# Performance work log

Measured on AMD Instinct MI355X. Metric: run time of the kernel, lower is better.

## Reference

```python
import jax, jax.numpy as jnp
import numpy as np

B, D, F, H = 256, 9, 8, 256   # batch of trees, tree depth, input features, hidden
N = 2 ** (D + 1) - 1          # total nodes per full binary tree (heap layout)


def _init(key, shape, fan_in):
    return jax.random.normal(key, shape, jnp.float32) * (1.0 / np.sqrt(fan_in))


def setup_inputs() -> dict:
    key = jax.random.key(0)
    ks = jax.random.split(key, 6)
    return {
        "data": jax.random.normal(ks[0], (B, N, F), jnp.float32),
        "Wu": _init(ks[1], (H, F), F),
        "bu": jnp.zeros((H,), jnp.float32),
        "Wr": _init(ks[2], (3 * H, 3 * H), 3 * H),
        "br": jnp.zeros((3 * H,), jnp.float32),
        "Wh": _init(ks[3], (H, 3 * H), 3 * H),
        "bh": jnp.zeros((H,), jnp.float32),
        "Wz": _init(ks[4], (4 * H, 4 * H), 4 * H),
        "bz": jnp.zeros((4 * H,), jnp.float32),
        "Wp": _init(ks[5], (1, H), H),
        "bp": jnp.zeros((1,), jnp.float32),
    }


def reference(data, Wu, bu, Wr, br, Wh, bh, Wz, bz, Wp, bp):
    # data: [B, N, F] node features in heap (level-order) layout;
    # children of the i-th node of level l are nodes 2i, 2i+1 of level l+1.
    b, n_nodes, _ = data.shape
    L = (n_nodes + 1) // 2          # number of leaves
    depth = L.bit_length() - 1
    h_dim = Wu.shape[0]

    # leaf embedding u for every node (leaf() is applied at every tree node)
    u = jnp.einsum('bnf,hf->bnh', data, Wu) + bu          # [B, N, H]
    h = u[:, L - 1:, :]                                    # leaf level states [B, L, H]

    for l in range(depth - 1, -1, -1):                     # bottom-up over levels
        n = 2 ** l
        parent = u[:, n - 1:2 * n - 1, :]                  # [B, n, H]
        h_l, h_r = h[:, 0::2, :], h[:, 1::2, :]            # [B, n, H] each
        hhu = jnp.concatenate([parent, h_l, h_r], axis=-1)  # [B, n, 3H]
        r = jax.nn.sigmoid(jnp.einsum('bnk,jk->bnj', hhu, Wr) + br)
        h_new = jax.nn.relu(jnp.einsum('bnk,hk->bnh', r * hhu, Wh) + bh)
        hhhu = jnp.concatenate([h_new, hhu], axis=-1)      # [B, n, 4H]
        zlin = jnp.einsum('bnk,jk->bnj', hhhu, Wz) + bz    # [B, n, 4H]
        z = jax.nn.softmax(zlin.reshape(b, n, 4, h_dim), axis=2)
        h = (z * hhhu.reshape(b, n, 4, h_dim)).sum(axis=2)  # gated combine -> [B, n, H]

    # h is [B, 1, H] at the root; logits head
    logits = jnp.einsum('bnh,oh->bno', h, Wp) + bp          # [B, 1, 1]
    return logits[:, 0, 0]                                  # [B]
```

## Files before the change

kernel.cpp:

```cpp
#include <hip/hip_runtime.h>
#include <math.h>

#define BB 256
#define NN 1023
#define FF 8
#define HH 256
#define DEPTH 9

enum { EPI_NONE = 0, EPI_SIGMUL = 1, EPI_RELU = 2, EPI_COMBINE = 3 };

typedef __bf16 bf16x8_t __attribute__((ext_vector_type(8)));
typedef float f32x4_t __attribute__((ext_vector_type(4)));

__device__ __forceinline__ void stage16(const void* g, void* l) {
    __builtin_amdgcn_global_load_lds(
        (const __attribute__((address_space(1))) void*)g,
        (__attribute__((address_space(3))) void*)l,
        16, 0, 0);
}

__device__ __forceinline__ int xcd_remap(int hw, int nwg) {
    const int xcd = hw & 7, k0 = hw >> 3;
    const int qq = nwg >> 3, rr = nwg & 7;
    return (xcd < rr ? xcd * (qq + 1) : rr * (qq + 1) + (xcd - rr) * qq) + k0;
}

template <int EPI>
__global__ __launch_bounds__(512, 1) void gemm256p(
    const __bf16* __restrict__ A, int lda,
    const __bf16* __restrict__ W,
    const float* __restrict__ bias,
    const __bf16* __restrict__ aux, int ldaux,
    void* __restrict__ Cout, int ldc,
    int K)
{
    __shared__ __bf16 lds[2][2][256 * 64];
    const int tid = threadIdx.x;
    const int lane = tid & 63;
    const int w = tid >> 6;
    const int wr = w >> 2, wc = w & 3;

    const int nwg = gridDim.x * gridDim.y;
    const int hw = blockIdx.y * gridDim.x + blockIdx.x;
    const int wg = xcd_remap(hw, nwg);
    const int bm0 = (wg / gridDim.x) * 256;
    const int bn0 = (wg % gridDim.x) * 256;

    const int srow = tid >> 3;
    const int scolz = ((tid & 7) ^ (srow & 7)) * 8;

    f32x4_t acc[8][4];
#pragma unroll
    for (int i = 0; i < 8; ++i)
#pragma unroll
        for (int j = 0; j < 4; ++j) acc[i][j] = (f32x4_t){0.f, 0.f, 0.f, 0.f};

    const int rA = lane & 15;
    const int klane = (lane >> 4) * 8;
    const int rxor = (lane & 7) * 8;
    const int NT = K >> 6;

#define STAGE_A_Q(t, buf, q)                                                   \
    do {                                                                       \
        const int kk_ = (t) << 6;                                              \
        stage16(A + (size_t)(bm0 + (q) * 64 + srow) * lda + kk_ + scolz,       \
                &lds[buf][0][((q) * 64) * 64 + w * 512]);                      \
        stage16(A + (size_t)(bm0 + 128 + (q) * 64 + srow) * lda + kk_ + scolz, \
                &lds[buf][0][((128 + (q) * 64)) * 64 + w * 512]);              \
    } while (0)
#define STAGE_B_H(t, buf, hf)                                                  \
    do {                                                                       \
        const int kk_ = (t) << 6;                                              \
        stage16(W + (size_t)(bn0 + (hf) * 128 + srow) * K + kk_ + scolz,       \
                &lds[buf][1][((hf) * 128) * 64 + w * 512]);                    \
        stage16(W + (size_t)(bn0 + (hf) * 128 + 64 + srow) * K + kk_ + scolz,  \
                &lds[buf][1][((hf) * 128 + 64) * 64 + w * 512]);               \
    } while (0)

#define LDA_F(As_, i, ks) \
    (*(const bf16x8_t*)&(As_)[(wr * 128 + (i) * 16 + rA) * 64 + (((ks) * 32 + klane) ^ rxor)])
#define LDB_F(Bs_, j, ks) \
    (*(const bf16x8_t*)&(Bs_)[(wc * 64 + (j) * 16 + rA) * 64 + (((ks) * 32 + klane) ^ rxor)])

    STAGE_A_Q(0, 0, 0);
    STAGE_B_H(0, 0, 0);
    STAGE_B_H(0, 0, 1);
    STAGE_A_Q(0, 0, 1);
    asm volatile("s_waitcnt vmcnt(2)" ::: "memory");
    __builtin_amdgcn_s_barrier();

    for (int t = 0; t < NT; ++t) {
        const int c = t & 1, n = c ^ 1;
        const __bf16* As = lds[c][0];
        const __bf16* Bs = lds[c][1];
        const bool more = (t + 1 < NT);
        bf16x8_t a0[4], a1[4], b0[4], b1[4];

#pragma unroll
        for (int j = 0; j < 4; ++j) b0[j] = LDB_F(Bs, j, 0);
#pragma unroll
        for (int i = 0; i < 4; ++i) a0[i] = LDA_F(As, i, 0);
        if (more) STAGE_A_Q(t + 1, n, 0);
        __builtin_amdgcn_s_barrier();
        asm volatile("s_waitcnt lgkmcnt(0)" ::: "memory");
        __builtin_amdgcn_s_setprio(1);
#pragma unroll
        for (int i = 0; i < 4; ++i)
#pragma unroll
            for (int j = 0; j < 4; ++j)
                acc[i][j] = __builtin_amdgcn_mfma_f32_16x16x32_bf16(
                    a0[i], b0[j], acc[i][j], 0, 0, 0);
        __builtin_amdgcn_s_setprio(0);
        __builtin_amdgcn_s_barrier();

#pragma unroll
        for (int j = 0; j < 4; ++j) b1[j] = LDB_F(Bs, j, 1);
#pragma unroll
        for (int i = 0; i < 4; ++i) a1[i] = LDA_F(As, i, 1);
        if (more) STAGE_B_H(t + 1, n, 0);
        __builtin_amdgcn_s_barrier();
        asm volatile("s_waitcnt lgkmcnt(0)" ::: "memory");
        __builtin_amdgcn_s_setprio(1);
#pragma unroll
        for (int i = 0; i < 4; ++i)
#pragma unroll
            for (int j = 0; j < 4; ++j)
                acc[i][j] = __builtin_amdgcn_mfma_f32_16x16x32_bf16(
                    a1[i], b1[j], acc[i][j], 0, 0, 0);
        __builtin_amdgcn_s_setprio(0);
        if (more) {
            asm volatile("s_waitcnt vmcnt(4)" ::: "memory");
        } else {
            asm volatile("s_waitcnt vmcnt(0)" ::: "memory");
        }
        __builtin_amdgcn_s_barrier();

#pragma unroll
        for (int i = 0; i < 4; ++i) a0[i] = LDA_F(As, 4 + i, 0);
        if (more) STAGE_B_H(t + 1, n, 1);
        __builtin_amdgcn_s_barrier();
        asm volatile("s_waitcnt lgkmcnt(0)" ::: "memory");
        __builtin_amdgcn_s_setprio(1);
#pragma unroll
        for (int i = 0; i < 4; ++i)
#pragma unroll
            for (int j = 0; j < 4; ++j)
                acc[4 + i][j] = __builtin_amdgcn_mfma_f32_16x16x32_bf16(
                    a0[i], b0[j], acc[4 + i][j], 0, 0, 0);
        __builtin_amdgcn_s_setprio(0);
        __builtin_amdgcn_s_barrier();

#pragma unroll
        for (int i = 0; i < 4; ++i) a1[i] = LDA_F(As, 4 + i, 1);
        if (more) STAGE_A_Q(t + 1, n, 1);
        __builtin_amdgcn_s_barrier();
        asm volatile("s_waitcnt lgkmcnt(0)" ::: "memory");
        __builtin_amdgcn_s_setprio(1);
#pragma unroll
        for (int i = 0; i < 4; ++i)
#pragma unroll
            for (int j = 0; j < 4; ++j)
                acc[4 + i][j] = __builtin_amdgcn_mfma_f32_16x16x32_bf16(
                    a1[i], b1[j], acc[4 + i][j], 0, 0, 0);
        __builtin_amdgcn_s_setprio(0);
        if (more) {
            asm volatile("s_waitcnt vmcnt(2)" ::: "memory");
            __builtin_amdgcn_s_barrier();
        }
    }
#undef STAGE_A_Q
#undef STAGE_B_H
#undef LDA_F
#undef LDB_F

    if (EPI == EPI_COMBINE) {
        const int r = lane & 15;
        const int G = ((bn0 + wc * 64) >> 2) + r;
        float bz4[4];
#pragma unroll
        for (int g = 0; g < 4; ++g) bz4[g] = bias[bn0 + wc * 64 + g * 16 + r];
#pragma unroll
        for (int i = 0; i < 8; ++i) {
#pragma unroll
            for (int reg = 0; reg < 4; ++reg) {
                const int gr = bm0 + wr * 128 + i * 16 + (lane >> 4) * 4 + reg;
                float z0 = acc[i][0][reg] + bz4[0];
                float z1 = acc[i][1][reg] + bz4[1];
                float z2 = acc[i][2][reg] + bz4[2];
                float z3 = acc[i][3][reg] + bz4[3];
                float mx = fmaxf(fmaxf(z0, z1), fmaxf(z2, z3));
                float e0 = __expf(z0 - mx), e1 = __expf(z1 - mx);
                float e2 = __expf(z2 - mx), e3 = __expf(z3 - mx);
                const __bf16* hrow = aux + (size_t)gr * ldaux + G;
                float hv = (e0 * (float)hrow[0] + e1 * (float)hrow[256] +
                            e2 * (float)hrow[512] + e3 * (float)hrow[768]) /
                           (e0 + e1 + e2 + e3);
                ((__bf16*)Cout)[(size_t)gr * ldc + G] = (__bf16)hv;
            }
        }
    } else {
#pragma unroll
        for (int j = 0; j < 4; ++j) {
            const int gc = bn0 + wc * 64 + j * 16 + (lane & 15);
            const float bv = bias[gc];
#pragma unroll
            for (int i = 0; i < 8; ++i) {
#pragma unroll
                for (int reg = 0; reg < 4; ++reg) {
                    const int gr = bm0 + wr * 128 + i * 16 + (lane >> 4) * 4 + reg;
                    float v = acc[i][j][reg] + bv;
                    if (EPI == EPI_SIGMUL) {
                        float s = 1.0f / (1.0f + __expf(-v));
                        v = s * (float)aux[(size_t)gr * ldaux + gc];
                        ((__bf16*)Cout)[(size_t)gr * ldc + gc] = (__bf16)v;
                    } else if (EPI == EPI_RELU) {
                        v = fmaxf(v, 0.0f);
                        ((__bf16*)Cout)[(size_t)gr * ldc + gc] = (__bf16)v;
                    } else {
                        ((float*)Cout)[(size_t)gr * ldc + gc] = v;
                    }
                }
            }
        }
    }
}

template <int EPI>
__global__ __launch_bounds__(256) void gemm_mfma(
    const __bf16* __restrict__ A, int lda,
    const __bf16* __restrict__ W,
    const float* __restrict__ bias,
    const __bf16* __restrict__ aux, int ldaux,
    void* __restrict__ Cout, int ldc,
    int K)
{
    __shared__ __bf16 As[128 * 32];
    __shared__ __bf16 Bs[128 * 32];
    const int tid = threadIdx.x;
    const int lane = tid & 63;
    const int w = tid >> 6;
    const int wr = w >> 1, wc = w & 1;

    const int nwg = gridDim.x * gridDim.y;
    const int hw = blockIdx.y * gridDim.x + blockIdx.x;
    const int wg = xcd_remap(hw, nwg);
    const int bm0 = (wg / gridDim.x) * 128;
    const int bn0 = (wg % gridDim.x) * 128;

    const int srow = lane >> 2;
    const int scol = (lane & 3) * 8;

    f32x4_t acc[4][4];
#pragma unroll
    for (int i = 0; i < 4; ++i)
#pragma unroll
        for (int j = 0; j < 4; ++j) acc[i][j] = (f32x4_t){0.f, 0.f, 0.f, 0.f};

    const int rA = lane & 15;
    const int kslot = (lane >> 4) * 8;

    for (int kk = 0; kk < K; kk += 32) {
        stage16(A + (size_t)(bm0 + w * 16 + srow) * lda + kk + scol,
                &As[(w * 16) * 32]);
        stage16(A + (size_t)(bm0 + 64 + w * 16 + srow) * lda + kk + scol,
                &As[(64 + w * 16) * 32]);
        stage16(W + (size_t)(bn0 + w * 16 + srow) * K + kk + scol,
                &Bs[(w * 16) * 32]);
        stage16(W + (size_t)(bn0 + 64 + w * 16 + srow) * K + kk + scol,
                &Bs[(64 + w * 16) * 32]);
        __syncthreads();

        bf16x8_t af[4], bfr[4];
#pragma unroll
        for (int i = 0; i < 4; ++i)
            af[i] = *(const bf16x8_t*)&As[(wr * 64 + i * 16 + rA) * 32 + kslot];
#pragma unroll
        for (int j = 0; j < 4; ++j)
            bfr[j] = *(const bf16x8_t*)&Bs[(wc * 64 + j * 16 + rA) * 32 + kslot];
#pragma unroll
        for (int i = 0; i < 4; ++i)
#pragma unroll
            for (int j = 0; j < 4; ++j)
                acc[i][j] = __builtin_amdgcn_mfma_f32_16x16x32_bf16(
                    af[i], bfr[j], acc[i][j], 0, 0, 0);
        __syncthreads();
    }

    if (EPI == EPI_COMBINE) {
        const int r = lane & 15;
        const int G = ((bn0 + wc * 64) >> 2) + r;
        float bz4[4];
#pragma unroll
        for (int g = 0; g < 4; ++g) bz4[g] = bias[bn0 + wc * 64 + g * 16 + r];
#pragma unroll
        for (int i = 0; i < 4; ++i) {
#pragma unroll
            for (int reg = 0; reg < 4; ++reg) {
                const int gr = bm0 + wr * 64 + i * 16 + (lane >> 4) * 4 + reg;
                float z0 = acc[i][0][reg] + bz4[0];
                float z1 = acc[i][1][reg] + bz4[1];
                float z2 = acc[i][2][reg] + bz4[2];
                float z3 = acc[i][3][reg] + bz4[3];
                float mx = fmaxf(fmaxf(z0, z1), fmaxf(z2, z3));
                float e0 = __expf(z0 - mx), e1 = __expf(z1 - mx);
                float e2 = __expf(z2 - mx), e3 = __expf(z3 - mx);
                const __bf16* hrow = aux + (size_t)gr * ldaux + G;
                float hv = (e0 * (float)hrow[0] + e1 * (float)hrow[256] +
                            e2 * (float)hrow[512] + e3 * (float)hrow[768]) /
                           (e0 + e1 + e2 + e3);
                ((__bf16*)Cout)[(size_t)gr * ldc + G] = (__bf16)hv;
            }
        }
    } else {
#pragma unroll
        for (int j = 0; j < 4; ++j) {
            const int gc = bn0 + wc * 64 + j * 16 + (lane & 15);
            const float bv = bias[gc];
#pragma unroll
            for (int i = 0; i < 4; ++i) {
#pragma unroll
                for (int reg = 0; reg < 4; ++reg) {
                    const int gr = bm0 + wr * 64 + i * 16 + (lane >> 4) * 4 + reg;
                    float v = acc[i][j][reg] + bv;
                    if (EPI == EPI_SIGMUL) {
                        float s = 1.0f / (1.0f + __expf(-v));
                        v = s * (float)aux[(size_t)gr * ldaux + gc];
                        ((__bf16*)Cout)[(size_t)gr * ldc + gc] = (__bf16)v;
                    } else if (EPI == EPI_RELU) {
                        v = fmaxf(v, 0.0f);
                        ((__bf16*)Cout)[(size_t)gr * ldc + gc] = (__bf16)v;
                    } else {
                        ((float*)Cout)[(size_t)gr * ldc + gc] = v;
                    }
                }
            }
        }
    }
}

__global__ __launch_bounds__(256) void convert_weights(
    const float* __restrict__ Wr, const float* __restrict__ Wh,
    const float* __restrict__ Wz, const float* __restrict__ bz,
    __bf16* __restrict__ Wrb, __bf16* __restrict__ Whb,
    __bf16* __restrict__ Wzb, float* __restrict__ bzp)
{
    const int NR = 768 * 768, NH2 = 256 * 768, NZ = 1024 * 1024;
    const int idx0 = blockIdx.x * 256 + threadIdx.x;
    for (int i = idx0; i < NR + NH2 + NZ; i += gridDim.x * 256) {
        if (i < NR) Wrb[i] = (__bf16)Wr[i];
        else if (i < NR + NH2) Whb[i - NR] = (__bf16)Wh[i - NR];
        else {
            const int z = i - NR - NH2;
            const int p = z >> 10, k = z & 1023;
            const int o = ((p >> 4) & 3) * 256 + (p >> 6) * 16 + (p & 15);
            Wzb[z] = (__bf16)Wz[(size_t)o * 1024 + k];
        }
    }
    if (idx0 < 1024) {
        const int p = idx0;
        const int o = ((p >> 4) & 3) * 256 + (p >> 6) * 16 + (p & 15);
        bzp[p] = bz[o];
    }
}

__global__ __launch_bounds__(256) void build_hhu(
    const float* __restrict__ data, const float* __restrict__ Wu,
    const float* __restrict__ bu, const __bf16* __restrict__ hprev,
    __bf16* __restrict__ hhhu, int l, int r0)
{
    const int n = 1 << l;
    const int blk = xcd_remap(blockIdx.x, gridDim.x);
    const int row = blk * 8 + (threadIdx.x >> 5);
    const int c0 = (threadIdx.x & 31) * 8;
    const int i = r0 + row;
    const int b = i >> l;
    const int m = i & (n - 1);

    float wv[8][8];
#pragma unroll
    for (int cc = 0; cc < 8; ++cc) {
        float4 w0 = *(const float4*)&Wu[(c0 + cc) * 8];
        float4 w1 = *(const float4*)&Wu[(c0 + cc) * 8 + 4];
        wv[cc][0] = w0.x; wv[cc][1] = w0.y; wv[cc][2] = w0.z; wv[cc][3] = w0.w;
        wv[cc][4] = w1.x; wv[cc][5] = w1.y; wv[cc][6] = w1.z; wv[cc][7] = w1.w;
    }
    float buv[8];
#pragma unroll
    for (int cc = 0; cc < 8; ++cc) buv[cc] = bu[c0 + cc];

    __bf16* rowp = hhhu + (size_t)row * 1024;

    {
        const float* dp = data + ((size_t)b * NN + (n - 1) + m) * FF;
        float4 d0 = *(const float4*)dp, d1 = *(const float4*)(dp + 4);
        float dv[8] = {d0.x, d0.y, d0.z, d0.w, d1.x, d1.y, d1.z, d1.w};
        bf16x8_t o;
#pragma unroll
        for (int cc = 0; cc < 8; ++cc) {
            float acc = buv[cc];
#pragma unroll
            for (int f = 0; f < 8; ++f) acc += dv[f] * wv[cc][f];
            o[cc] = (__bf16)acc;
        }
        *(bf16x8_t*)&rowp[256 + c0] = o;
    }

    if (l == 8) {
        const float* dl = data + ((size_t)b * NN + 511 + 2 * m) * FF;
#pragma unroll
        for (int side = 0; side < 2; ++side) {
            const float* dp = dl + side * FF;
            float4 d0 = *(const float4*)dp, d1 = *(const float4*)(dp + 4);
            float dv[8] = {d0.x, d0.y, d0.z, d0.w, d1.x, d1.y, d1.z, d1.w};
            bf16x8_t o;
#pragma unroll
            for (int cc = 0; cc < 8; ++cc) {
                float acc = buv[cc];
#pragma unroll
                for (int f = 0; f < 8; ++f) acc += dv[f] * wv[cc][f];
                o[cc] = (__bf16)acc;
            }
            *(bf16x8_t*)&rowp[512 + side * 256 + c0] = o;
        }
    } else {
        *(bf16x8_t*)&rowp[512 + c0] =
            *(const bf16x8_t*)&hprev[((size_t)b * (2 * n) + 2 * m) * HH + c0];
        *(bf16x8_t*)&rowp[768 + c0] =
            *(const bf16x8_t*)&hprev[((size_t)b * (2 * n) + 2 * m + 1) * HH + c0];
    }
}

__global__ __launch_bounds__(256) void final_kernel(
    const __bf16* __restrict__ hfin, const float* __restrict__ Wp,
    const float* __restrict__ bp, float* __restrict__ out)
{
    const int b = blockIdx.x;
    const int t = threadIdx.x;
    __shared__ float red[256];
    red[t] = (float)hfin[(size_t)b * HH + t] * Wp[t];
    __syncthreads();
    for (int s = 128; s > 0; s >>= 1) {
        if (t < s) red[t] += red[t + s];
        __syncthreads();
    }
    if (t == 0) out[b] = red[0] + bp[0];
}

extern "C" void kernel_launch(void* const* d_in, const int* in_sizes, int n_in,
                              void* d_out, int out_size, void* d_ws, size_t ws_size,
                              hipStream_t stream)
{
    const float* data = (const float*)d_in[0];
    const float* Wu = (const float*)d_in[1];
    const float* bu = (const float*)d_in[2];
    const float* Wr = (const float*)d_in[3];
    const float* br = (const float*)d_in[4];
    const float* Wh = (const float*)d_in[5];
    const float* bh = (const float*)d_in[6];
    const float* Wz = (const float*)d_in[7];
    const float* bz = (const float*)d_in[8];
    const float* Wp = (const float*)d_in[9];
    const float* bp = (const float*)d_in[10];
    float* out = (float*)d_out;

    const size_t CAP = 32768;
    char* w = (char*)d_ws;
    __bf16* hA = (__bf16*)w;   w += (size_t)65536 * HH * 2;
    __bf16* hB = (__bf16*)w;   w += (size_t)32768 * HH * 2;
    __bf16* hhhu = (__bf16*)w; w += CAP * 1024 * 2;
    __bf16* rh = (__bf16*)w;   w += CAP * 768 * 2;
    __bf16* Wrb = (__bf16*)w;  w += (size_t)768 * 768 * 2;
    __bf16* Whb = (__bf16*)w;  w += (size_t)256 * 768 * 2;
    __bf16* Wzb = (__bf16*)w;  w += (size_t)1024 * 1024 * 2;
    float* bzp = (float*)w;    w += 1024 * 4;

    convert_weights<<<2048, 256, 0, stream>>>(Wr, Wh, Wz, bz, Wrb, Whb, Wzb, bzp);

    for (int l = DEPTH - 1; l >= 0; --l) {
        const size_t M = (size_t)BB << l;
        __bf16* dst = ((DEPTH - 1 - l) & 1) ? hB : hA;
        const __bf16* src = ((DEPTH - 1 - l) & 1) ? hA : hB;
        for (size_t r0 = 0; r0 < M; r0 += CAP) {
            const int R = (int)((M - r0 < CAP) ? (M - r0) : CAP);
            build_hhu<<<R / 8, 256, 0, stream>>>(data, Wu, bu, src, hhhu, l, (int)r0);
            if (R >= 2048) {
                gemm256p<EPI_SIGMUL><<<dim3(3, R / 256), 512, 0, stream>>>(
                    hhhu + 256, 1024, Wrb, br, hhhu + 256, 1024, rh, 768, 768);
            } else {
                gemm_mfma<EPI_SIGMUL><<<dim3(6, R / 128), 256, 0, stream>>>(
                    hhhu + 256, 1024, Wrb, br, hhhu + 256, 1024, rh, 768, 768);
            }
            gemm_mfma<EPI_RELU><<<dim3(2, R / 128), 256, 0, stream>>>(
                rh, 768, Whb, bh, nullptr, 0, hhhu, 1024, 768);
            if (R >= 2048) {
                gemm256p<EPI_COMBINE><<<dim3(4, R / 256), 512, 0, stream>>>(
                    hhhu, 1024, Wzb, bzp, hhhu, 1024,
                    dst + (size_t)r0 * HH, HH, 1024);
            } else {
                gemm_mfma<EPI_COMBINE><<<dim3(8, R / 128), 256, 0, stream>>>(
                    hhhu, 1024, Wzb, bzp, hhhu, 1024,
                    dst + (size_t)r0 * HH, HH, 1024);
            }
        }
    }
    final_kernel<<<BB, 256, 0, stream>>>(hA, Wp, bp, out);
}
```

Measured before the change: 1.250 ms.

## Fold Wu into Wr/Wz and gather GEMM A-operands directly from tree buffers

Precomputes folded weights so the parent-embedding term of the reset and gate GEMMs uses the 8 raw bf16 input features, padded to 64, instead of the 256-wide u vector. This cuts K from 768 to 576 and from 1024 to 832. The large-level GEMMs now gather A tiles straight from child hidden states, converted data and the new-h buffer, so the concatenated hhhu buffer is no longer built. Small levels keep the old path. The cost is irregular gather addressing and an extra bf16 rounding of the folded weights.

```diff
diff --git a/kernel.cpp b/kernel.cpp
--- a/kernel.cpp
+++ b/kernel.cpp
@@ -26,13 +26,34 @@
 }
 
 template <int EPI>
-__global__ __launch_bounds__(512, 1) void gemm256p(
-    const __bf16* __restrict__ A, int lda,
+__device__ __forceinline__ const __bf16* a_src(
+    int t, size_t gi, int l, int lrow, int scolz,
+    const __bf16* __restrict__ hprev, const __bf16* __restrict__ hnew,
+    const __bf16* __restrict__ dbf)
+{
+    const int b = (int)(gi >> l);
+    const int m = (int)gi & ((1 << l) - 1);
+    const size_t child = (((size_t)b) << (l + 1)) + 2 * m;
+    if (EPI == EPI_SIGMUL) {
+        if (t == 0) return dbf + ((size_t)b * NN + (1 << l) - 1 + m) * FF;
+        if (t <= 4) return hprev + child * HH + (t - 1) * 64 + scolz;
+        return hprev + (child + 1) * HH + (t - 5) * 64 + scolz;
+    } else {
+        if (t < 4) return hnew + (size_t)lrow * HH + t * 64 + scolz;
+        if (t == 4) return dbf + ((size_t)b * NN + (1 << l) - 1 + m) * FF;
+        if (t <= 8) return hprev + child * HH + (t - 5) * 64 + scolz;
+        return hprev + (child + 1) * HH + (t - 9) * 64 + scolz;
+    }
+}
+
+template <int EPI>
+__global__ __launch_bounds__(512, 1) void gemm256g(
+    const __bf16* __restrict__ hprev, const __bf16* __restrict__ ubuf,
+    const __bf16* __restrict__ hnew, const __bf16* __restrict__ dbf,
     const __bf16* __restrict__ W,
     const float* __restrict__ bias,
-    const __bf16* __restrict__ aux, int ldaux,
-    void* __restrict__ Cout, int ldc,
-    int K)
+    void* __restrict__ Cout,
+    int r0, int l, int K)
 {
     __shared__ __bf16 lds[2][2][256 * 64];
     const int tid = threadIdx.x;
@@ -48,6 +69,7 @@
 
     const int srow = tid >> 3;
     const int scolz = ((tid & 7) ^ (srow & 7)) * 8;
+    const int mask = (1 << l) - 1;
 
     f32x4_t acc[8][4];
 #pragma unroll
@@ -60,13 +82,17 @@
     const int rxor = (lane & 7) * 8;
     const int NT = K >> 6;
 
+#define STAGE_A_LINE(t, buf, rbase)                                            \
+    do {                                                                       \
+        const int lrow_ = bm0 + (rbase) + srow;                                \
+        const __bf16* s_ = a_src<EPI>((t), (size_t)r0 + lrow_, l, lrow_,       \
+                                      scolz, hprev, hnew, dbf);                \
+        stage16(s_, &lds[buf][0][(rbase) * 64 + w * 512]);                     \
+    } while (0)
 #define STAGE_A_Q(t, buf, q)                                                   \
     do {                                                                       \
-        const int kk_ = (t) << 6;                                              \
-        stage16(A + (size_t)(bm0 + (q) * 64 + srow) * lda + kk_ + scolz,       \
-                &lds[buf][0][((q) * 64) * 64 + w * 512]);                      \
-        stage16(A + (size_t)(bm0 + 128 + (q) * 64 + srow) * lda + kk_ + scolz, \
-                &lds[buf][0][((128 + (q) * 64)) * 64 + w * 512]);              \
+        STAGE_A_LINE(t, buf, (q) * 64);                                        \
+        STAGE_A_LINE(t, buf, 128 + (q) * 64);                                  \
     } while (0)
 #define STAGE_B_H(t, buf, hf)                                                  \
     do {                                                                       \
@@ -76,7 +102,6 @@
         stage16(W + (size_t)(bn0 + (hf) * 128 + 64 + srow) * K + kk_ + scolz,  \
                 &lds[buf][1][((hf) * 128 + 64) * 64 + w * 512]);               \
     } while (0)
-
 #define LDA_F(As_, i, ks) \
     (*(const bf16x8_t*)&(As_)[(wr * 128 + (i) * 16 + rA) * 64 + (((ks) * 32 + klane) ^ rxor)])
 #define LDB_F(Bs_, j, ks) \
@@ -90,7 +115,7 @@
     __builtin_amdgcn_s_barrier();
 
     for (int t = 0; t < NT; ++t) {
-        const int c = t & 1, n = c ^ 1;
+        const int c = t & 1, nb = c ^ 1;
         const __bf16* As = lds[c][0];
         const __bf16* Bs = lds[c][1];
         const bool more = (t + 1 < NT);
@@ -100,7 +125,7 @@
         for (int j = 0; j < 4; ++j) b0[j] = LDB_F(Bs, j, 0);
 #pragma unroll
         for (int i = 0; i < 4; ++i) a0[i] = LDA_F(As, i, 0);
-        if (more) STAGE_A_Q(t + 1, n, 0);
+        if (more) STAGE_A_Q(t + 1, nb, 0);
         __builtin_amdgcn_s_barrier();
         asm volatile("s_waitcnt lgkmcnt(0)" ::: "memory");
         __builtin_amdgcn_s_setprio(1);
@@ -117,7 +142,7 @@
         for (int j = 0; j < 4; ++j) b1[j] = LDB_F(Bs, j, 1);
 #pragma unroll
         for (int i = 0; i < 4; ++i) a1[i] = LDA_F(As, i, 1);
-        if (more) STAGE_B_H(t + 1, n, 0);
+        if (more) STAGE_B_H(t + 1, nb, 0);
         __builtin_amdgcn_s_barrier();
         asm volatile("s_waitcnt lgkmcnt(0)" ::: "memory");
         __builtin_amdgcn_s_setprio(1);
@@ -137,7 +162,7 @@
 
 #pragma unroll
         for (int i = 0; i < 4; ++i) a0[i] = LDA_F(As, 4 + i, 0);
-        if (more) STAGE_B_H(t + 1, n, 1);
+        if (more) STAGE_B_H(t + 1, nb, 1);
         __builtin_amdgcn_s_barrier();
         asm volatile("s_waitcnt lgkmcnt(0)" ::: "memory");
         __builtin_amdgcn_s_setprio(1);
@@ -152,7 +177,7 @@
 
 #pragma unroll
         for (int i = 0; i < 4; ++i) a1[i] = LDA_F(As, 4 + i, 1);
-        if (more) STAGE_A_Q(t + 1, n, 1);
+        if (more) STAGE_A_Q(t + 1, nb, 1);
         __builtin_amdgcn_s_barrier();
         asm volatile("s_waitcnt lgkmcnt(0)" ::: "memory");
         __builtin_amdgcn_s_setprio(1);
@@ -168,13 +193,40 @@
             __builtin_amdgcn_s_barrier();
         }
     }
+#undef STAGE_A_LINE
 #undef STAGE_A_Q
 #undef STAGE_B_H
 #undef LDA_F
 #undef LDB_F
 
-    if (EPI == EPI_COMBINE) {
-        const int r = lane & 15;
+    const int hi = lane >> 4;
+    const int r = lane & 15;
+
+    if (EPI == EPI_SIGMUL) {
+#pragma unroll
+        for (int j = 0; j < 4; ++j) {
+            const int gc = bn0 + wc * 64 + j * 16 + r;
+            const float bv = bias[gc];
+#pragma unroll
+            for (int i = 0; i < 8; ++i) {
+#pragma unroll
+                for (int reg = 0; reg < 4; ++reg) {
+                    const int gr = bm0 + wr * 128 + i * 16 + hi * 4 + reg;
+                    const size_t gi = (size_t)r0 + gr;
+                    const int b = (int)(gi >> l);
+                    const int m = (int)gi & mask;
+                    const size_t child = (((size_t)b) << (l + 1)) + 2 * m;
+                    float a;
+                    if (gc < 256) a = (float)ubuf[(size_t)gr * HH + gc];
+                    else if (gc < 512) a = (float)hprev[child * HH + gc - 256];
+                    else a = (float)hprev[(child + 1) * HH + gc - 512];
+                    float v = acc[i][j][reg] + bv;
+                    float s = 1.0f / (1.0f + __expf(-v));
+                    ((__bf16*)Cout)[(size_t)gr * 768 + gc] = (__bf16)(s * a);
+                }
+            }
+        }
+    } else {
         const int G = ((bn0 + wc * 64) >> 2) + r;
         float bz4[4];
 #pragma unroll
@@ -183,7 +235,11 @@
         for (int i = 0; i < 8; ++i) {
 #pragma unroll
             for (int reg = 0; reg < 4; ++reg) {
-                const int gr = bm0 + wr * 128 + i * 16 + (lane >> 4) * 4 + reg;
+                const int gr = bm0 + wr * 128 + i * 16 + hi * 4 + reg;
+                const size_t gi = (size_t)r0 + gr;
+                const int b = (int)(gi >> l);
+                const int m = (int)gi & mask;
+                const size_t child = (((size_t)b) << (l + 1)) + 2 * m;
                 float z0 = acc[i][0][reg] + bz4[0];
                 float z1 = acc[i][1][reg] + bz4[1];
                 float z2 = acc[i][2][reg] + bz4[2];
@@ -191,35 +247,13 @@
                 float mx = fmaxf(fmaxf(z0, z1), fmaxf(z2, z3));
                 float e0 = __expf(z0 - mx), e1 = __expf(z1 - mx);
                 float e2 = __expf(z2 - mx), e3 = __expf(z3 - mx);
-                const __bf16* hrow = aux + (size_t)gr * ldaux + G;
-                float hv = (e0 * (float)hrow[0] + e1 * (float)hrow[256] +
-                            e2 * (float)hrow[512] + e3 * (float)hrow[768]) /
+                float a0v = (float)hnew[(size_t)gr * HH + G];
+                float a1v = (float)ubuf[(size_t)gr * HH + G];
+                float a2v = (float)hprev[child * HH + G];
+                float a3v = (float)hprev[(child + 1) * HH + G];
+                float hv = (e0 * a0v + e1 * a1v + e2 * a2v + e3 * a3v) /
                            (e0 + e1 + e2 + e3);
-                ((__bf16*)Cout)[(size_t)gr * ldc + G] = (__bf16)hv;
-            }
-        }
-    } else {
-#pragma unroll
-        for (int j = 0; j < 4; ++j) {
-            const int gc = bn0 + wc * 64 + j * 16 + (lane & 15);
-            const float bv = bias[gc];
-#pragma unroll
-            for (int i = 0; i < 8; ++i) {
-#pragma unroll
-                for (int reg = 0; reg < 4; ++reg) {
-                    const int gr = bm0 + wr * 128 + i * 16 + (lane >> 4) * 4 + reg;
-                    float v = acc[i][j][reg] + bv;
-                    if (EPI == EPI_SIGMUL) {
-                        float s = 1.0f / (1.0f + __expf(-v));
-                        v = s * (float)aux[(size_t)gr * ldaux + gc];
-                        ((__bf16*)Cout)[(size_t)gr * ldc + gc] = (__bf16)v;
-                    } else if (EPI == EPI_RELU) {
-                        v = fmaxf(v, 0.0f);
-                        ((__bf16*)Cout)[(size_t)gr * ldc + gc] = (__bf16)v;
-                    } else {
-                        ((float*)Cout)[(size_t)gr * ldc + gc] = v;
-                    }
-                }
+                ((__bf16*)Cout)[gi * HH + G] = (__bf16)hv;
             }
         }
     }
@@ -363,18 +397,76 @@
     }
 }
 
-__global__ __launch_bounds__(256) void build_hhu(
+__global__ __launch_bounds__(256) void conv_data(
+    const float* __restrict__ data, __bf16* __restrict__ dbf)
+{
+    const int N = BB * NN * FF;
+    for (int i = blockIdx.x * 256 + threadIdx.x; i < N; i += gridDim.x * 256)
+        dbf[i] = (__bf16)data[i];
+}
+
+__global__ __launch_bounds__(256) void fold_wr(
+    const float* __restrict__ Wr, const float* __restrict__ Wu,
+    const float* __restrict__ bu, const float* __restrict__ br,
+    __bf16* __restrict__ Wrp, float* __restrict__ brp)
+{
+    const int j = blockIdx.x;
+    const int c = threadIdx.x;
+    __shared__ float red[256];
+    const float wjc = Wr[(size_t)j * 768 + c];
+    red[c] = wjc * bu[c];
+    __syncthreads();
+    for (int s = 128; s > 0; s >>= 1) { if (c < s) red[c] += red[c + s]; __syncthreads(); }
+    if (c == 0) brp[j] = br[j] + red[0];
+    for (int f = 0; f < 8; ++f) {
+        __syncthreads();
+        red[c] = wjc * Wu[c * 8 + f];
+        __syncthreads();
+        for (int s = 128; s > 0; s >>= 1) { if (c < s) red[c] += red[c + s]; __syncthreads(); }
+        if (c == 0) Wrp[(size_t)j * 576 + f] = (__bf16)red[0];
+    }
+    if (c >= 8 && c < 64) Wrp[(size_t)j * 576 + c] = (__bf16)0.0f;
+    Wrp[(size_t)j * 576 + 64 + c]  = (__bf16)Wr[(size_t)j * 768 + 256 + c];
+    Wrp[(size_t)j * 576 + 320 + c] = (__bf16)Wr[(size_t)j * 768 + 512 + c];
+}
+
+__global__ __launch_bounds__(256) void fold_wz(
+    const float* __restrict__ Wz, const float* __restrict__ Wu,
+    const float* __restrict__ bu, const float* __restrict__ bz,
+    __bf16* __restrict__ Wzp, float* __restrict__ bzpf)
+{
+    const int p = blockIdx.x;
+    const int c = threadIdx.x;
+    const int o = ((p >> 4) & 3) * 256 + (p >> 6) * 16 + (p & 15);
+    __shared__ float red[256];
+    const float wuc = Wz[(size_t)o * 1024 + 256 + c];
+    red[c] = wuc * bu[c];
+    __syncthreads();
+    for (int s = 128; s > 0; s >>= 1) { if (c < s) red[c] += red[c + s]; __syncthreads(); }
+    if (c == 0) bzpf[p] = bz[o] + red[0];
+    for (int f = 0; f < 8; ++f) {
+        __syncthreads();
+        red[c] = wuc * Wu[c * 8 + f];
+        __syncthreads();
+        for (int s = 128; s > 0; s >>= 1) { if (c < s) red[c] += red[c + s]; __syncthreads(); }
+        if (c == 0) Wzp[(size_t)p * 832 + 256 + f] = (__bf16)red[0];
+    }
+    if (c >= 8 && c < 64) Wzp[(size_t)p * 832 + 256 + c] = (__bf16)0.0f;
+    Wzp[(size_t)p * 832 + c]       = (__bf16)Wz[(size_t)o * 1024 + c];
+    Wzp[(size_t)p * 832 + 320 + c] = (__bf16)Wz[(size_t)o * 1024 + 512 + c];
+    Wzp[(size_t)p * 832 + 576 + c] = (__bf16)Wz[(size_t)o * 1024 + 768 + c];
+}
+
+__global__ __launch_bounds__(256) void build_u(
     const float* __restrict__ data, const float* __restrict__ Wu,
-    const float* __restrict__ bu, const __bf16* __restrict__ hprev,
-    __bf16* __restrict__ hhhu, int l, int r0)
+    const float* __restrict__ bu, __bf16* __restrict__ out, int l, int r0)
 {
     const int n = 1 << l;
-    const int blk = xcd_remap(blockIdx.x, gridDim.x);
-    const int row = blk * 8 + (threadIdx.x >> 5);
+    const int row = blockIdx.x * 8 + (threadIdx.x >> 5);
     const int c0 = (threadIdx.x & 31) * 8;
-    const int i = r0 + row;
-    const int b = i >> l;
-    const int m = i & (n - 1);
+    const size_t i = (size_t)r0 + row;
+    const int b = (int)(i >> l);
+    const int m = (int)i & (n - 1);
 
     float wv[8][8];
 #pragma unroll
@@ -384,50 +476,57 @@
         wv[cc][0] = w0.x; wv[cc][1] = w0.y; wv[cc][2] = w0.z; wv[cc][3] = w0.w;
         wv[cc][4] = w1.x; wv[cc][5] = w1.y; wv[cc][6] = w1.z; wv[cc][7] = w1.w;
     }
-    float buv[8];
-#pragma unroll
-    for (int cc = 0; cc < 8; ++cc) buv[cc] = bu[c0 + cc];
-
+    const float* dp = data + ((size_t)b * NN + (n - 1) + m) * FF;
+    float4 d0 = *(const float4*)dp, d1 = *(const float4*)(dp + 4);
+    float dv[8] = {d0.x, d0.y, d0.z, d0.w, d1.x, d1.y, d1.z, d1.w};
+    bf16x8_t o;
+#pragma unroll
+    for (int cc = 0; cc < 8; ++cc) {
+        float acc = bu[c0 + cc];
+#pragma unroll
+        for (int f = 0; f < 8; ++f) acc += dv[f] * wv[cc][f];
+        o[cc] = (__bf16)acc;
+    }
+    *(bf16x8_t*)&out[(size_t)row * HH + c0] = o;
+}
+
+__global__ __launch_bounds__(256) void build_hhu(
+    const float* __restrict__ data, const float* __restrict__ Wu,
+    const float* __restrict__ bu, const __bf16* __restrict__ hprev,
+    __bf16* __restrict__ hhhu, int l, int r0)
+{
+    const int n = 1 << l;
+    const int row = blockIdx.x * 8 + (threadIdx.x >> 5);
+    const int c0 = (threadIdx.x & 31) * 8;
+    const int i = r0 + row;
+    const int b = i >> l;
+    const int m = i & (n - 1);
+
+    float wv[8][8];
+#pragma unroll
+    for (int cc = 0; cc < 8; ++cc) {
+        float4 w0 = *(const float4*)&Wu[(c0 + cc) * 8];
+        float4 w1 = *(const float4*)&Wu[(c0 + cc) * 8 + 4];
+        wv[cc][0] = w0.x; wv[cc][1] = w0.y; wv[cc][2] = w0.z; wv[cc][3] = w0.w;
+        wv[cc][4] = w1.x; wv[cc][5] = w1.y; wv[cc][6] = w1.z; wv[cc][7] = w1.w;
+    }
+    const float* dp = data + ((size_t)b * NN + (n - 1) + m) * FF;
+    float4 d0 = *(const float4*)dp, d1 = *(const float4*)(dp + 4);
+    float dv[8] = {d0.x, d0.y, d0.z, d0.w, d1.x, d1.y, d1.z, d1.w};
     __bf16* rowp = hhhu + (size_t)row * 1024;
-
-    {
-        const float* dp = data + ((size_t)b * NN + (n - 1) + m) * FF;
-        float4 d0 = *(const float4*)dp, d1 = *(const float4*)(dp + 4);
-        float dv[8] = {d0.x, d0.y, d0.z, d0.w, d1.x, d1.y, d1.z, d1.w};
-        bf16x8_t o;
-#pragma unroll
-        for (int cc = 0; cc < 8; ++cc) {
-            float acc = buv[cc];
-#pragma unroll
-            for (int f = 0; f < 8; ++f) acc += dv[f] * wv[cc][f];
-            o[cc] = (__bf16)acc;
-        }
-        *(bf16x8_t*)&rowp[256 + c0] = o;
-    }
-
-    if (l == 8) {
-        const float* dl = data + ((size_t)b * NN + 511 + 2 * m) * FF;
-#pragma unroll
-        for (int side = 0; side < 2; ++side) {
-            const float* dp = dl + side * FF;
-            float4 d0 = *(const float4*)dp, d1 = *(const float4*)(dp + 4);
-            float dv[8] = {d0.x, d0.y, d0.z, d0.w, d1.x, d1.y, d1.z, d1.w};
-            bf16x8_t o;
-#pragma unroll
-            for (int cc = 0; cc < 8; ++cc) {
-                float acc = buv[cc];
-#pragma unroll
-                for (int f = 0; f < 8; ++f) acc += dv[f] * wv[cc][f];
-                o[cc] = (__bf16)acc;
-            }
-            *(bf16x8_t*)&rowp[512 + side * 256 + c0] = o;
-        }
-    } else {
-        *(bf16x8_t*)&rowp[512 + c0] =
-            *(const bf16x8_t*)&hprev[((size_t)b * (2 * n) + 2 * m) * HH + c0];
-        *(bf16x8_t*)&rowp[768 + c0] =
-            *(const bf16x8_t*)&hprev[((size_t)b * (2 * n) + 2 * m + 1) * HH + c0];
-    }
+    bf16x8_t o;
+#pragma unroll
+    for (int cc = 0; cc < 8; ++cc) {
+        float acc = bu[c0 + cc];
+#pragma unroll
+        for (int f = 0; f < 8; ++f) acc += dv[f] * wv[cc][f];
+        o[cc] = (__bf16)acc;
+    }
+    *(bf16x8_t*)&rowp[256 + c0] = o;
+    *(bf16x8_t*)&rowp[512 + c0] =
+        *(const bf16x8_t*)&hprev[((size_t)b * (2 * n) + 2 * m) * HH + c0];
+    *(bf16x8_t*)&rowp[768 + c0] =
+        *(const bf16x8_t*)&hprev[((size_t)b * (2 * n) + 2 * m + 1) * HH + c0];
 }
 
 __global__ __launch_bounds__(256) void final_kernel(
@@ -465,43 +564,58 @@
 
     const size_t CAP = 32768;
     char* w = (char*)d_ws;
-    __bf16* hA = (__bf16*)w;   w += (size_t)65536 * HH * 2;
-    __bf16* hB = (__bf16*)w;   w += (size_t)32768 * HH * 2;
-    __bf16* hhhu = (__bf16*)w; w += CAP * 1024 * 2;
-    __bf16* rh = (__bf16*)w;   w += CAP * 768 * 2;
-    __bf16* Wrb = (__bf16*)w;  w += (size_t)768 * 768 * 2;
-    __bf16* Whb = (__bf16*)w;  w += (size_t)256 * 768 * 2;
-    __bf16* Wzb = (__bf16*)w;  w += (size_t)1024 * 1024 * 2;
-    float* bzp = (float*)w;    w += 1024 * 4;
+    __bf16* leafU = (__bf16*)w; w += (size_t)131072 * HH * 2;
+    __bf16* hA = (__bf16*)w;    w += (size_t)65536 * HH * 2;
+    __bf16* hB = (__bf16*)w;    w += (size_t)32768 * HH * 2;
+    __bf16* ubuf = (__bf16*)w;  w += CAP * HH * 2;
+    __bf16* hnewb = (__bf16*)w; w += CAP * HH * 2;
+    __bf16* rh = (__bf16*)w;    w += CAP * 768 * 2;
+    __bf16* dbf = (__bf16*)w;   w += (size_t)BB * NN * FF * 2;
+    __bf16* hhhuS = (__bf16*)w; w += (size_t)1024 * 1024 * 2;
+    __bf16* Wrb = (__bf16*)w;   w += (size_t)768 * 768 * 2;
+    __bf16* Whb = (__bf16*)w;   w += (size_t)256 * 768 * 2;
+    __bf16* Wzb = (__bf16*)w;   w += (size_t)1024 * 1024 * 2;
+    float* bzp = (float*)w;     w += 1024 * 4;
+    __bf16* Wrp = (__bf16*)w;   w += (size_t)768 * 576 * 2;
+    float* brp = (float*)w;     w += 768 * 4;
+    __bf16* Wzp = (__bf16*)w;   w += (size_t)1024 * 832 * 2;
+    float* bzpf = (float*)w;    w += 1024 * 4;
 
     convert_weights<<<2048, 256, 0, stream>>>(Wr, Wh, Wz, bz, Wrb, Whb, Wzb, bzp);
-
-    for (int l = DEPTH - 1; l >= 0; --l) {
+    conv_data<<<1024, 256, 0, stream>>>(data, dbf);
+    fold_wr<<<768, 256, 0, stream>>>(Wr, Wu, bu, br, Wrp, brp);
+    fold_wz<<<1024, 256, 0, stream>>>(Wz, Wu, bu, bz, Wzp, bzpf);
+    build_u<<<131072 / 8, 256, 0, stream>>>(data, Wu, bu, leafU, 9, 0);
+
+    const __bf16* src = leafU;
+    __bf16* dst = hA;
+    __bf16* other = hB;
+    for (int l = DEPTH - 1; l >= 3; --l) {
         const size_t M = (size_t)BB << l;
-        __bf16* dst = ((DEPTH - 1 - l) & 1) ? hB : hA;
-        const __bf16* src = ((DEPTH - 1 - l) & 1) ? hA : hB;
         for (size_t r0 = 0; r0 < M; r0 += CAP) {
             const int R = (int)((M - r0 < CAP) ? (M - r0) : CAP);
-            build_hhu<<<R / 8, 256, 0, stream>>>(data, Wu, bu, src, hhhu, l, (int)r0);
-            if (R >= 2048) {
-                gemm256p<EPI_SIGMUL><<<dim3(3, R / 256), 512, 0, stream>>>(
-                    hhhu + 256, 1024, Wrb, br, hhhu + 256, 1024, rh, 768, 768);
-            } else {
-                gemm_mfma<EPI_SIGMUL><<<dim3(6, R / 128), 256, 0, stream>>>(
-                    hhhu + 256, 1024, Wrb, br, hhhu + 256, 1024, rh, 768, 768);
-            }
+            build_u<<<R / 8, 256, 0, stream>>>(data, Wu, bu, ubuf, l, (int)r0);
+            gemm256g<EPI_SIGMUL><<<dim3(3, R / 256), 512, 0, stream>>>(
+                src, ubuf, nullptr, dbf, Wrp, brp, rh, (int)r0, l, 576);
             gemm_mfma<EPI_RELU><<<dim3(2, R / 128), 256, 0, stream>>>(
-                rh, 768, Whb, bh, nullptr, 0, hhhu, 1024, 768);
-            if (R >= 2048) {
-                gemm256p<EPI_COMBINE><<<dim3(4, R / 256), 512, 0, stream>>>(
-                    hhhu, 1024, Wzb, bzp, hhhu, 1024,
-                    dst + (size_t)r0 * HH, HH, 1024);
-            } else {
-                gemm_mfma<EPI_COMBINE><<<dim3(8, R / 128), 256, 0, stream>>>(
-                    hhhu, 1024, Wzb, bzp, hhhu, 1024,
-                    dst + (size_t)r0 * HH, HH, 1024);
-            }
-        }
-    }
-    final_kernel<<<BB, 256, 0, stream>>>(hA, Wp, bp, out);
-}
+                rh, 768, Whb, bh, nullptr, 0, hnewb, 256, 768);
+            gemm256g<EPI_COMBINE><<<dim3(4, R / 256), 512, 0, stream>>>(
+                src, ubuf, hnewb, dbf, Wzp, bzpf, dst, (int)r0, l, 832);
+        }
+        src = dst;
+        __bf16* t2 = dst; dst = other; other = t2;
+    }
+    for (int l = 2; l >= 0; --l) {
+        const int R = BB << l;
+        build_hhu<<<R / 8, 256, 0, stream>>>(data, Wu, bu, src, hhhuS, l, 0);
+        gemm_mfma<EPI_SIGMUL><<<dim3(6, R / 128), 256, 0, stream>>>(
+            hhhuS + 256, 1024, Wrb, br, hhhuS + 256, 1024, rh, 768, 768);
+        gemm_mfma<EPI_RELU><<<dim3(2, R / 128), 256, 0, stream>>>(
+            rh, 768, Whb, bh, nullptr, 0, hhhuS, 1024, 768);
+        gemm_mfma<EPI_COMBINE><<<dim3(8, R / 128), 256, 0, stream>>>(
+            hhhuS, 1024, Wzb, bzp, hhhuS, 1024, dst, HH, 1024);
+        src = dst;
+        __bf16* t2 = dst; dst = other; other = t2;
+    }
+    final_kernel<<<BB, 256, 0, stream>>>(src, Wp, bp, out);
+}
```

New measurement: 1.610 ms. +28.7%, slower.
